# Kernel tuning notes

Measured on AMD Instinct MI355X. Metric: run time of the kernel, lower is better.

## Reference

```python
import jax, jax.numpy as jnp
import numpy as np

B, T, IN, H = 4096, 128, 768, 256


def setup_inputs() -> dict:
    key = jax.random.key(0)
    ks = jax.random.split(key, 5)
    s1 = 1.0 / np.sqrt(IN)
    s2 = 1.0 / np.sqrt(H)
    return {
        "x": jax.random.normal(ks[0], (B, IN), jnp.float32),
        "W1": jax.random.normal(ks[1], (T, IN, H), jnp.float32) * s1,
        "b1": jnp.zeros((T, H), jnp.float32),
        "W2": jax.random.normal(ks[2], (T, H, H), jnp.float32) * s2,
        "b2": jnp.zeros((T, H), jnp.float32),
        "W3": jax.random.normal(ks[3], (T, H), jnp.float32) * s2,
        "b3": jnp.zeros((T,), jnp.float32),
    }


def reference(x, W1, b1, W2, b2, W3, b3):
    # Per-task 3-layer MLP, vectorized over tasks. Dropout is eval-mode (identity).
    h = jax.nn.relu(jnp.einsum('bi,tih->bth', x, W1) + b1)          # [B, T, H]
    h = jax.nn.relu(jnp.einsum('bth,thk->btk', h, W2) + b2)         # [B, T, H]
    out = jnp.einsum('bth,th->bt', h, W3) + b3                      # [B, T]
    return out
```

## Files before the change

kernel.cpp:

```cpp
#include <hip/hip_runtime.h>
#include <cstdint>
#include <cstddef>

#define B_   4096
#define T_   128
#define IN_  768
#define H_   256
#define BM_  256
#define KC1  (IN_ / 32)
#define KC2  (H_ / 32)

typedef __bf16 bf16_t;
typedef bf16_t bf16x8 __attribute__((ext_vector_type(8)));
typedef bf16_t bf16x4 __attribute__((ext_vector_type(4)));
typedef float  floatx16 __attribute__((ext_vector_type(16)));

#define MFMA32(a, b, c) __builtin_amdgcn_mfma_f32_32x32x16_bf16((a), (b), (c), 0, 0, 0)

#define WAITBAR(N) asm volatile("s_waitcnt vmcnt(" #N ") lgkmcnt(0)\n\ts_barrier" ::: "memory")
#define WAIT_LGK_BAR() asm volatile("s_waitcnt lgkmcnt(0)\n\ts_barrier" ::: "memory")

__device__ __forceinline__ void gl_lds16(const bf16_t* g, bf16_t* l) {
    __builtin_amdgcn_global_load_lds(
        (const __attribute__((address_space(1))) void*)g,
        (__attribute__((address_space(3))) void*)l, 16, 0, 0);
}

__device__ __forceinline__ void tile_w_body(const float* __restrict__ src,
                                            bf16_t* __restrict__ dst,
                                            int K, int KC, int blk) {
    const int t  = blk / KC;
    const int kc = blk - t * KC;
    const int kq = threadIdx.x >> 6;
    const int h4 = (threadIdx.x & 63) * 4;
    const float* s = src + ((size_t)t * K + kc * 32 + kq * 8) * H_ + h4;
    float r[8][4];
#pragma unroll
    for (int e = 0; e < 8; ++e) {
        float4 v = *(const float4*)(s + (size_t)e * H_);
        r[e][0] = v.x; r[e][1] = v.y; r[e][2] = v.z; r[e][3] = v.w;
    }
    bf16_t* d = dst + (((size_t)(t * KC + kc) * 4 + kq) * H_ + h4) * 8;
#pragma unroll
    for (int c = 0; c < 4; ++c) {
        bf16x8 v;
#pragma unroll
        for (int e = 0; e < 8; ++e) v[e] = (bf16_t)r[e][c];
        *(bf16x8*)(d + c * 8) = v;
    }
}

__device__ __forceinline__ void tile_x_body(const float* __restrict__ src,
                                            bf16_t* __restrict__ dst, long long o) {
    int m = (int)(o & 127);
    long long q = o >> 7;
    int kq = (int)(q & 3);
    int q2 = (int)(q >> 2);
    int kc   = q2 % KC1;
    int mblk = q2 / KC1;
    const float* s = src + ((long long)mblk * 128 + m) * IN_ + kc * 32 + kq * 8;
    float4 a = *(const float4*)s;
    float4 b = *(const float4*)(s + 4);
    bf16x8 v;
    v[0] = (bf16_t)a.x; v[1] = (bf16_t)a.y; v[2] = (bf16_t)a.z; v[3] = (bf16_t)a.w;
    v[4] = (bf16_t)b.x; v[5] = (bf16_t)b.y; v[6] = (bf16_t)b.z; v[7] = (bf16_t)b.w;
    *(bf16x8*)(dst + o * 8) = v;
}

__global__ __launch_bounds__(256)
void prep_all(const float* __restrict__ x,  bf16_t* __restrict__ xt,
              const float* __restrict__ W1, bf16_t* __restrict__ w1t,
              const float* __restrict__ W2, bf16_t* __restrict__ w2t) {
    const int b = blockIdx.x;
    if (b < 1536) {
        long long o = (long long)b * 256 + threadIdx.x;
        tile_x_body(x, xt, o);
    } else if (b < 1536 + 3072) {
        tile_w_body(W1, w1t, IN_, KC1, b - 1536);
    } else {
        tile_w_body(W2, w2t, H_, KC2, b - 4608);
    }
}

__global__ __launch_bounds__(512, 2)
void mtmlp_fused5(const bf16_t* __restrict__ xt, const bf16_t* __restrict__ w1t,
                  const float* __restrict__ b1, const bf16_t* __restrict__ w2t,
                  const float* __restrict__ b2, const float* __restrict__ W3,
                  const float* __restrict__ b3, float* __restrict__ out) {
    const int L    = blockIdx.x;
    const int xcd  = L & 7;
    const int slot = L >> 3;
    const int t    = xcd * 16 + (slot >> 4);
    const int mblk = slot & 15;
    const int m0   = mblk * BM_;
    const int mb0  = mblk * 2;

    const int tid  = threadIdx.x;
    const int lane = tid & 63;
    const int wid  = tid >> 6;
    const int wm   = wid >> 2;
    const int wn   = wid & 3;
    const int ln31 = lane & 31;
    const int hi   = lane >> 5;

    __shared__ __align__(16) bf16_t hbuf[BM_ * H_];
    __shared__ __align__(16) bf16_t wt2[2 * 4 * H_ * 8];
    float* w3s = (float*)wt2;

    floatx16 acc[4][2];
#pragma unroll
    for (int i = 0; i < 4; ++i)
#pragma unroll
        for (int j = 0; j < 2; ++j)
#pragma unroll
            for (int e = 0; e < 16; ++e) acc[i][j][e] = 0.0f;

    const bf16_t* w1base = w1t + (size_t)t * KC1 * 8192;
    const bf16_t* w2base = w2t + (size_t)t * KC2 * 8192;
    const bf16_t* xw = xt + (size_t)(mb0 + (wn >> 1)) * KC1 * 4096;
    const int lbase = hi * 1024 + (wn & 1) * 512 + ln31 * 8;
    const int abase = hi * 2048 + wm * 1024 + ln31 * 8;

    bf16_t* const sl0 = hbuf;
    bf16_t* const sl1 = hbuf + 8192;
    bf16_t* const sl2 = hbuf + 16384;
    bf16_t* const sl3 = hbuf + 24576;

    auto stageW = [&](bf16_t* dst, int kc) {
        const bf16_t* ws = w1base + (size_t)kc * 8192;
        gl_lds16(ws + tid * 8,        dst + tid * 8);
        gl_lds16(ws + 4096 + tid * 8, dst + 4096 + tid * 8);
    };
    auto stage2 = [&](bf16_t* dst, int kc) {
        const bf16_t* ws = w2base + (size_t)kc * 8192;
        gl_lds16(ws + tid * 8,        dst + tid * 8);
        gl_lds16(ws + 4096 + tid * 8, dst + 4096 + tid * 8);
    };

#define LOADX(XV, kcc) do {                                          \
        const bf16_t* xp_ = xw + (size_t)(kcc) * 4096;               \
        XV##0 = *(const bf16x8*)(xp_ + lbase + 0 * 2048 + 0 * 256);  \
        XV##1 = *(const bf16x8*)(xp_ + lbase + 0 * 2048 + 1 * 256);  \
        XV##2 = *(const bf16x8*)(xp_ + lbase + 1 * 2048 + 0 * 256);  \
        XV##3 = *(const bf16x8*)(xp_ + lbase + 1 * 2048 + 1 * 256);  \
    } while (0)

#define COMP1(bp_, XV) do {                                          \
        const bf16_t* b_ = (bp_);                                    \
        bf16x8 A0_, A1_, A2_, A3_;                                   \
        A0_ = *(const bf16x8*)(b_ + abase + 0 * 4096 + 0 * 256);     \
        A1_ = *(const bf16x8*)(b_ + abase + 0 * 4096 + 1 * 256);     \
        A2_ = *(const bf16x8*)(b_ + abase + 0 * 4096 + 2 * 256);     \
        A3_ = *(const bf16x8*)(b_ + abase + 0 * 4096 + 3 * 256);     \
        acc[0][0] = MFMA32(A0_, XV##0, acc[0][0]);                   \
        acc[0][1] = MFMA32(A0_, XV##1, acc[0][1]);                   \
        acc[1][0] = MFMA32(A1_, XV##0, acc[1][0]);                   \
        acc[1][1] = MFMA32(A1_, XV##1, acc[1][1]);                   \
        acc[2][0] = MFMA32(A2_, XV##0, acc[2][0]);                   \
        acc[2][1] = MFMA32(A2_, XV##1, acc[2][1]);                   \
        acc[3][0] = MFMA32(A3_, XV##0, acc[3][0]);                   \
        acc[3][1] = MFMA32(A3_, XV##1, acc[3][1]);                   \
        A0_ = *(const bf16x8*)(b_ + abase + 1 * 4096 + 0 * 256);     \
        A1_ = *(const bf16x8*)(b_ + abase + 1 * 4096 + 1 * 256);     \
        A2_ = *(const bf16x8*)(b_ + abase + 1 * 4096 + 2 * 256);     \
        A3_ = *(const bf16x8*)(b_ + abase + 1 * 4096 + 3 * 256);     \
        acc[0][0] = MFMA32(A0_, XV##2, acc[0][0]);                   \
        acc[0][1] = MFMA32(A0_, XV##3, acc[0][1]);                   \
        acc[1][0] = MFMA32(A1_, XV##2, acc[1][0]);                   \
        acc[1][1] = MFMA32(A1_, XV##3, acc[1][1]);                   \
        acc[2][0] = MFMA32(A2_, XV##2, acc[2][0]);                   \
        acc[2][1] = MFMA32(A2_, XV##3, acc[2][1]);                   \
        acc[3][0] = MFMA32(A3_, XV##2, acc[3][0]);                   \
        acc[3][1] = MFMA32(A3_, XV##3, acc[3][1]);                   \
    } while (0)

    bf16x8 xA0, xA1, xA2, xA3, xB0, xB1, xB2, xB3;

    stageW(sl0, 0); stageW(sl1, 1); stageW(sl2, 2);
    LOADX(xA, 0); LOADX(xB, 1);

    WAITBAR(4); stageW(sl3, 3); COMP1(sl0, xA); LOADX(xA, 2);
    WAITBAR(6); stageW(sl0, 4); COMP1(sl1, xB); LOADX(xB, 3);
    WAITBAR(6); stageW(sl1, 5); COMP1(sl2, xA); LOADX(xA, 4);
    WAITBAR(6); stageW(sl2, 6); COMP1(sl3, xB); LOADX(xB, 5);

    for (int q = 1; q <= 4; ++q) {
        const int kc = q * 4;
        WAITBAR(6); stageW(sl3, kc + 3); COMP1(sl0, xA); LOADX(xA, kc + 2);
        WAITBAR(6); stageW(sl0, kc + 4); COMP1(sl1, xB); LOADX(xB, kc + 3);
        WAITBAR(6); stageW(sl1, kc + 5); COMP1(sl2, xA); LOADX(xA, kc + 4);
        WAITBAR(6); stageW(sl2, kc + 6); COMP1(sl3, xB); LOADX(xB, kc + 5);
    }
    WAITBAR(6); stageW(sl3, 23); COMP1(sl0, xA); LOADX(xA, 22);
    WAITBAR(6);                  COMP1(sl1, xB); LOADX(xB, 23);
    WAITBAR(4); stage2(wt2, 0); stage2(wt2 + 8192, 1); COMP1(sl2, xA);
    WAITBAR(4);                  COMP1(sl3, xB);
    WAIT_LGK_BAR();

#pragma unroll
    for (int i = 0; i < 4; ++i) {
#pragma unroll
        for (int g = 0; g < 4; ++g) {
            const int h0 = wm * 128 + i * 32 + g * 8 + 4 * hi;
            float4 bias = *(const float4*)(b1 + t * H_ + h0);
            const int blk = h0 >> 3;
#pragma unroll
            for (int j = 0; j < 2; ++j) {
                const int mm = wn * 64 + j * 32 + ln31;
                bf16x4 o;
                o[0] = (bf16_t)fmaxf(acc[i][j][4 * g + 0] + bias.x, 0.0f);
                o[1] = (bf16_t)fmaxf(acc[i][j][4 * g + 1] + bias.y, 0.0f);
                o[2] = (bf16_t)fmaxf(acc[i][j][4 * g + 2] + bias.z, 0.0f);
                o[3] = (bf16_t)fmaxf(acc[i][j][4 * g + 3] + bias.w, 0.0f);
                *(bf16x4*)(hbuf + (size_t)(blk * BM_ + mm) * 8 + 4 * hi) = o;
            }
        }
    }

#pragma unroll
    for (int i = 0; i < 4; ++i)
#pragma unroll
        for (int j = 0; j < 2; ++j)
#pragma unroll
            for (int e = 0; e < 16; ++e) acc[i][j][e] = 0.0f;

    auto comp2 = [&](const bf16_t* wbuf, int kc) {
#pragma unroll
        for (int s = 0; s < 2; ++s) {
            const int kq = s * 2 + hi;
            bf16x8 A[4], Bf[2];
#pragma unroll
            for (int i = 0; i < 4; ++i)
                A[i] = *(const bf16x8*)(wbuf + (size_t)(kq * H_ + wm * 128 + i * 32 + ln31) * 8);
            const int blk = kc * 4 + kq;
#pragma unroll
            for (int j = 0; j < 2; ++j) {
                const int mm = wn * 64 + j * 32 + ln31;
                Bf[j] = *(const bf16x8*)(hbuf + (size_t)(blk * BM_ + mm) * 8);
            }
#pragma unroll
            for (int i = 0; i < 4; ++i)
#pragma unroll
                for (int j = 0; j < 2; ++j) acc[i][j] = MFMA32(A[i], Bf[j], acc[i][j]);
        }
    };

    for (int kc = 0; kc < KC2; ++kc) {
        if (kc < KC2 - 1) { WAITBAR(2); } else { WAITBAR(0); }
        comp2(wt2 + (kc & 1) * 8192, kc);
        WAIT_LGK_BAR();
        if (kc < KC2 - 2) stage2(wt2 + (kc & 1) * 8192, kc + 2);
    }

    if (tid < H_) w3s[tid] = W3[t * H_ + tid];
#pragma unroll
    for (int i = 0; i < 4; ++i) {
#pragma unroll
        for (int g = 0; g < 4; ++g) {
            const int h0 = wm * 128 + i * 32 + g * 8 + 4 * hi;
            float4 bias = *(const float4*)(b2 + t * H_ + h0);
            const int blk = h0 >> 3;
#pragma unroll
            for (int j = 0; j < 2; ++j) {
                const int mm = wn * 64 + j * 32 + ln31;
                bf16x4 o;
                o[0] = (bf16_t)fmaxf(acc[i][j][4 * g + 0] + bias.x, 0.0f);
                o[1] = (bf16_t)fmaxf(acc[i][j][4 * g + 1] + bias.y, 0.0f);
                o[2] = (bf16_t)fmaxf(acc[i][j][4 * g + 2] + bias.z, 0.0f);
                o[3] = (bf16_t)fmaxf(acc[i][j][4 * g + 3] + bias.w, 0.0f);
                *(bf16x4*)(hbuf + (size_t)(blk * BM_ + mm) * 8 + 4 * hi) = o;
            }
        }
    }
    WAIT_LGK_BAR();

    {
        const int m = tid >> 1, seg = tid & 1;
        float sum = 0.0f;
#pragma unroll
        for (int b = 0; b < 16; ++b) {
            const int blk = seg * 16 + b;
            const bf16x8 v = *(const bf16x8*)(hbuf + (size_t)(blk * BM_ + m) * 8);
            const float* w = w3s + blk * 8;
#pragma unroll
            for (int e = 0; e < 8; ++e) sum += (float)v[e] * w[e];
        }
        sum += __shfl_xor(sum, 1);
        if (seg == 0) out[(size_t)(m0 + m) * T_ + t] = sum + b3[t];
    }
#undef LOADX
#undef COMP1
}

extern "C" void kernel_launch(void* const* d_in, const int* in_sizes, int n_in,
                              void* d_out, int out_size, void* d_ws, size_t ws_size,
                              hipStream_t stream) {
    const float* x  = (const float*)d_in[0];
    const float* W1 = (const float*)d_in[1];
    const float* b1 = (const float*)d_in[2];
    const float* W2 = (const float*)d_in[3];
    const float* b2 = (const float*)d_in[4];
    const float* W3 = (const float*)d_in[5];
    const float* b3 = (const float*)d_in[6];
    float* out = (float*)d_out;

    const size_t nx  = (size_t)B_ * IN_;
    const size_t nw1 = (size_t)T_ * IN_ * H_;

    bf16_t* xt  = (bf16_t*)d_ws;
    bf16_t* w1t = xt + nx;
    bf16_t* w2t = w1t + nw1;

    prep_all<<<dim3(5632), 256, 0, stream>>>(x, xt, W1, w1t, W2, w2t);
    mtmlp_fused5<<<dim3(2048), 512, 0, stream>>>(xt, w1t, b1, w2t, b2, W3, b3, out);
}
```

Before: 456.8 us.

## Restage layer-1 W1 in paired triple buffers and stream layer-2 weights from registers

Layer 1 now stages two K-chunks of W1 per step into three 16K-element LDS slots (P0/P1/P2), so there are half as many barriers per K. Layer 2 no longer stages W2 through LDS. Each wave loads its own W2 fragments straight from global into double-buffered registers, and only the hidden activations are read from LDS. This removes the separate wt2 LDS buffer and the barriers around it, which shrinks LDS use. The cost is more registers and global-load latency that is no longer hidden behind barriers, plus less prefetch lead in layer 1.

Result: slower. 488.0 us (+6.8%).

```diff
diff --git a/kernel.cpp b/kernel.cpp
--- a/kernel.cpp
+++ b/kernel.cpp
@@ -83,7 +83,7 @@
 }
 
 __global__ __launch_bounds__(512, 2)
-void mtmlp_fused5(const bf16_t* __restrict__ xt, const bf16_t* __restrict__ w1t,
+void mtmlp_fused6(const bf16_t* __restrict__ xt, const bf16_t* __restrict__ w1t,
                   const float* __restrict__ b1, const bf16_t* __restrict__ w2t,
                   const float* __restrict__ b2, const float* __restrict__ W3,
                   const float* __restrict__ b3, float* __restrict__ out) {
@@ -104,8 +104,7 @@
     const int hi   = lane >> 5;
 
     __shared__ __align__(16) bf16_t hbuf[BM_ * H_];
-    __shared__ __align__(16) bf16_t wt2[2 * 4 * H_ * 8];
-    float* w3s = (float*)wt2;
+    __shared__ float w3s[H_];
 
     floatx16 acc[4][2];
 #pragma unroll
@@ -120,21 +119,19 @@
     const bf16_t* xw = xt + (size_t)(mb0 + (wn >> 1)) * KC1 * 4096;
     const int lbase = hi * 1024 + (wn & 1) * 512 + ln31 * 8;
     const int abase = hi * 2048 + wm * 1024 + ln31 * 8;
-
-    bf16_t* const sl0 = hbuf;
-    bf16_t* const sl1 = hbuf + 8192;
-    bf16_t* const sl2 = hbuf + 16384;
-    bf16_t* const sl3 = hbuf + 24576;
-
-    auto stageW = [&](bf16_t* dst, int kc) {
+    const int mm0 = wn * 64 + ln31;
+    const int mm1 = mm0 + 32;
+
+    bf16_t* const P0 = hbuf;
+    bf16_t* const P1 = hbuf + 16384;
+    bf16_t* const P2 = hbuf + 32768;
+
+    auto stageWpair = [&](bf16_t* dst, int kc) {
         const bf16_t* ws = w1base + (size_t)kc * 8192;
-        gl_lds16(ws + tid * 8,        dst + tid * 8);
-        gl_lds16(ws + 4096 + tid * 8, dst + 4096 + tid * 8);
-    };
-    auto stage2 = [&](bf16_t* dst, int kc) {
-        const bf16_t* ws = w2base + (size_t)kc * 8192;
-        gl_lds16(ws + tid * 8,        dst + tid * 8);
-        gl_lds16(ws + 4096 + tid * 8, dst + 4096 + tid * 8);
+        gl_lds16(ws + tid * 8,         dst + tid * 8);
+        gl_lds16(ws + 4096 + tid * 8,  dst + 4096 + tid * 8);
+        gl_lds16(ws + 8192 + tid * 8,  dst + 8192 + tid * 8);
+        gl_lds16(ws + 12288 + tid * 8, dst + 12288 + tid * 8);
     };
 
 #define LOADX(XV, kcc) do {                                          \
@@ -174,27 +171,35 @@
         acc[3][1] = MFMA32(A3_, XV##3, acc[3][1]);                   \
     } while (0)
 
-    bf16x8 xA0, xA1, xA2, xA3, xB0, xB1, xB2, xB3;
-
-    stageW(sl0, 0); stageW(sl1, 1); stageW(sl2, 2);
-    LOADX(xA, 0); LOADX(xB, 1);
-
-    WAITBAR(4); stageW(sl3, 3); COMP1(sl0, xA); LOADX(xA, 2);
-    WAITBAR(6); stageW(sl0, 4); COMP1(sl1, xB); LOADX(xB, 3);
-    WAITBAR(6); stageW(sl1, 5); COMP1(sl2, xA); LOADX(xA, 4);
-    WAITBAR(6); stageW(sl2, 6); COMP1(sl3, xB); LOADX(xB, 5);
-
-    for (int q = 1; q <= 4; ++q) {
-        const int kc = q * 4;
-        WAITBAR(6); stageW(sl3, kc + 3); COMP1(sl0, xA); LOADX(xA, kc + 2);
-        WAITBAR(6); stageW(sl0, kc + 4); COMP1(sl1, xB); LOADX(xB, kc + 3);
-        WAITBAR(6); stageW(sl1, kc + 5); COMP1(sl2, xA); LOADX(xA, kc + 4);
-        WAITBAR(6); stageW(sl2, kc + 6); COMP1(sl3, xB); LOADX(xB, kc + 5);
-    }
-    WAITBAR(6); stageW(sl3, 23); COMP1(sl0, xA); LOADX(xA, 22);
-    WAITBAR(6);                  COMP1(sl1, xB); LOADX(xB, 23);
-    WAITBAR(4); stage2(wt2, 0); stage2(wt2 + 8192, 1); COMP1(sl2, xA);
-    WAITBAR(4);                  COMP1(sl3, xB);
+#define SUPER(CB, WB, XUa, XUb, XNa, XNb, c) do {                    \
+        WAITBAR(4);                                                  \
+        LOADX(XNa, (c) + 2); LOADX(XNb, (c) + 3);                    \
+        stageWpair(WB, (c) + 4);                                     \
+        COMP1(CB, XUa); COMP1((CB) + 8192, XUb);                     \
+    } while (0)
+
+    bf16x8 xPA0, xPA1, xPA2, xPA3, xPB0, xPB1, xPB2, xPB3;
+    bf16x8 xQA0, xQA1, xQA2, xQA3, xQB0, xQB1, xQB2, xQB3;
+
+    LOADX(xPA, 0); LOADX(xPB, 1);
+    stageWpair(P0, 0);
+    stageWpair(P1, 2);
+
+    SUPER(P0, P2, xPA, xPB, xQA, xQB, 0);
+    SUPER(P1, P0, xQA, xQB, xPA, xPB, 2);
+    SUPER(P2, P1, xPA, xPB, xQA, xQB, 4);
+    SUPER(P0, P2, xQA, xQB, xPA, xPB, 6);
+    SUPER(P1, P0, xPA, xPB, xQA, xQB, 8);
+    SUPER(P2, P1, xQA, xQB, xPA, xPB, 10);
+    SUPER(P0, P2, xPA, xPB, xQA, xQB, 12);
+    SUPER(P1, P0, xQA, xQB, xPA, xPB, 14);
+    SUPER(P2, P1, xPA, xPB, xQA, xQB, 16);
+    SUPER(P0, P2, xQA, xQB, xPA, xPB, 18);
+    WAITBAR(4);
+    LOADX(xQA, 22); LOADX(xQB, 23);
+    COMP1(P1, xPA); COMP1(P1 + 8192, xPB);
+    WAITBAR(0);
+    COMP1(P2, xQA); COMP1(P2 + 8192, xQB);
     WAIT_LGK_BAR();
 
 #pragma unroll
@@ -224,33 +229,61 @@
 #pragma unroll
             for (int e = 0; e < 16; ++e) acc[i][j][e] = 0.0f;
 
-    auto comp2 = [&](const bf16_t* wbuf, int kc) {
-#pragma unroll
-        for (int s = 0; s < 2; ++s) {
-            const int kq = s * 2 + hi;
-            bf16x8 A[4], Bf[2];
-#pragma unroll
-            for (int i = 0; i < 4; ++i)
-                A[i] = *(const bf16x8*)(wbuf + (size_t)(kq * H_ + wm * 128 + i * 32 + ln31) * 8);
-            const int blk = kc * 4 + kq;
-#pragma unroll
-            for (int j = 0; j < 2; ++j) {
-                const int mm = wn * 64 + j * 32 + ln31;
-                Bf[j] = *(const bf16x8*)(hbuf + (size_t)(blk * BM_ + mm) * 8);
-            }
-#pragma unroll
-            for (int i = 0; i < 4; ++i)
-#pragma unroll
-                for (int j = 0; j < 2; ++j) acc[i][j] = MFMA32(A[i], Bf[j], acc[i][j]);
-        }
-    };
-
-    for (int kc = 0; kc < KC2; ++kc) {
-        if (kc < KC2 - 1) { WAITBAR(2); } else { WAITBAR(0); }
-        comp2(wt2 + (kc & 1) * 8192, kc);
-        WAIT_LGK_BAR();
-        if (kc < KC2 - 2) stage2(wt2 + (kc & 1) * 8192, kc + 2);
-    }
+    WAIT_LGK_BAR();
+
+#define LOADW2(WV, kcc) do {                                         \
+        const bf16_t* wp_ = w2base + (size_t)(kcc) * 8192;           \
+        WV##0 = *(const bf16x8*)(wp_ + abase + 0 * 4096 + 0 * 256);  \
+        WV##1 = *(const bf16x8*)(wp_ + abase + 0 * 4096 + 1 * 256);  \
+        WV##2 = *(const bf16x8*)(wp_ + abase + 0 * 4096 + 2 * 256);  \
+        WV##3 = *(const bf16x8*)(wp_ + abase + 0 * 4096 + 3 * 256);  \
+        WV##4 = *(const bf16x8*)(wp_ + abase + 1 * 4096 + 0 * 256);  \
+        WV##5 = *(const bf16x8*)(wp_ + abase + 1 * 4096 + 1 * 256);  \
+        WV##6 = *(const bf16x8*)(wp_ + abase + 1 * 4096 + 2 * 256);  \
+        WV##7 = *(const bf16x8*)(wp_ + abase + 1 * 4096 + 3 * 256);  \
+    } while (0)
+
+#define COMP2R(WV, kcc) do {                                         \
+        bf16x8 B0_, B1_;                                             \
+        const int blkA_ = (kcc) * 4 + hi;                            \
+        B0_ = *(const bf16x8*)(hbuf + (size_t)(blkA_ * BM_ + mm0) * 8); \
+        B1_ = *(const bf16x8*)(hbuf + (size_t)(blkA_ * BM_ + mm1) * 8); \
+        acc[0][0] = MFMA32(WV##0, B0_, acc[0][0]);                   \
+        acc[0][1] = MFMA32(WV##0, B1_, acc[0][1]);                   \
+        acc[1][0] = MFMA32(WV##1, B0_, acc[1][0]);                   \
+        acc[1][1] = MFMA32(WV##1, B1_, acc[1][1]);                   \
+        acc[2][0] = MFMA32(WV##2, B0_, acc[2][0]);                   \
+        acc[2][1] = MFMA32(WV##2, B1_, acc[2][1]);                   \
+        acc[3][0] = MFMA32(WV##3, B0_, acc[3][0]);                   \
+        acc[3][1] = MFMA32(WV##3, B1_, acc[3][1]);                   \
+        const int blkB_ = (kcc) * 4 + 2 + hi;                        \
+        B0_ = *(const bf16x8*)(hbuf + (size_t)(blkB_ * BM_ + mm0) * 8); \
+        B1_ = *(const bf16x8*)(hbuf + (size_t)(blkB_ * BM_ + mm1) * 8); \
+        acc[0][0] = MFMA32(WV##4, B0_, acc[0][0]);                   \
+        acc[0][1] = MFMA32(WV##4, B1_, acc[0][1]);                   \
+        acc[1][0] = MFMA32(WV##5, B0_, acc[1][0]);                   \
+        acc[1][1] = MFMA32(WV##5, B1_, acc[1][1]);                   \
+        acc[2][0] = MFMA32(WV##6, B0_, acc[2][0]);                   \
+        acc[2][1] = MFMA32(WV##6, B1_, acc[2][1]);                   \
+        acc[3][0] = MFMA32(WV##7, B0_, acc[3][0]);                   \
+        acc[3][1] = MFMA32(WV##7, B1_, acc[3][1]);                   \
+    } while (0)
+
+    {
+        bf16x8 wa0, wa1, wa2, wa3, wa4, wa5, wa6, wa7;
+        bf16x8 wb0, wb1, wb2, wb3, wb4, wb5, wb6, wb7;
+        LOADW2(wa, 0); LOADW2(wb, 1);
+        COMP2R(wa, 0); LOADW2(wa, 2);
+        COMP2R(wb, 1); LOADW2(wb, 3);
+        COMP2R(wa, 2); LOADW2(wa, 4);
+        COMP2R(wb, 3); LOADW2(wb, 5);
+        COMP2R(wa, 4); LOADW2(wa, 6);
+        COMP2R(wb, 5); LOADW2(wb, 7);
+        COMP2R(wa, 6);
+        COMP2R(wb, 7);
+    }
+
+    WAIT_LGK_BAR();
 
     if (tid < H_) w3s[tid] = W3[t * H_ + tid];
 #pragma unroll
@@ -290,6 +323,9 @@
     }
 #undef LOADX
 #undef COMP1
+#undef SUPER
+#undef LOADW2
+#undef COMP2R
 }
 
 extern "C" void kernel_launch(void* const* d_in, const int* in_sizes, int n_in,
@@ -312,5 +348,5 @@
     bf16_t* w2t = w1t + nw1;
 
     prep_all<<<dim3(5632), 256, 0, stream>>>(x, xt, W1, w1t, W2, w2t);
-    mtmlp_fused5<<<dim3(2048), 512, 0, stream>>>(xt, w1t, b1, w2t, b2, W3, b3, out);
-}
+    mtmlp_fused6<<<dim3(2048), 512, 0, stream>>>(xt, w1t, b1, w2t, b2, W3, b3, out);
+}
```

## Halve batch tile to 128, raise occupancy, stream W2 directly into registers

Applied to the files above, without the earlier changes.

Shrinks the per-block batch tile from 256 to 128 rows, doubling the grid and halving the accumulator registers so launch bounds can request four blocks per SIMD. The second-layer weights are now loaded straight from global memory into registers with double-buffering, instead of being staged through an LDS double buffer. The final dot product is split four ways per row. In exchange, each W1/W2 tile is fetched twice as often per batch row, and the register path for W2 loses the LDS sharing across waves.

Measured after the change: 484.0 us. 1.06x slower.

```diff
diff --git a/kernel.cpp b/kernel.cpp
--- a/kernel.cpp
+++ b/kernel.cpp
@@ -6,7 +6,7 @@
 #define T_   128
 #define IN_  768
 #define H_   256
-#define BM_  256
+#define BM_  128
 #define KC1  (IN_ / 32)
 #define KC2  (H_ / 32)
 
@@ -82,18 +82,17 @@
     }
 }
 
-__global__ __launch_bounds__(512, 2)
-void mtmlp_fused5(const bf16_t* __restrict__ xt, const bf16_t* __restrict__ w1t,
+__global__ __launch_bounds__(512, 4)
+void mtmlp_fused7(const bf16_t* __restrict__ xt, const bf16_t* __restrict__ w1t,
                   const float* __restrict__ b1, const bf16_t* __restrict__ w2t,
                   const float* __restrict__ b2, const float* __restrict__ W3,
                   const float* __restrict__ b3, float* __restrict__ out) {
     const int L    = blockIdx.x;
     const int xcd  = L & 7;
     const int slot = L >> 3;
-    const int t    = xcd * 16 + (slot >> 4);
-    const int mblk = slot & 15;
+    const int t    = xcd * 16 + (slot >> 5);
+    const int mblk = slot & 31;
     const int m0   = mblk * BM_;
-    const int mb0  = mblk * 2;
 
     const int tid  = threadIdx.x;
     const int lane = tid & 63;
@@ -104,22 +103,20 @@
     const int hi   = lane >> 5;
 
     __shared__ __align__(16) bf16_t hbuf[BM_ * H_];
-    __shared__ __align__(16) bf16_t wt2[2 * 4 * H_ * 8];
-    float* w3s = (float*)wt2;
-
-    floatx16 acc[4][2];
+    __shared__ float w3s[H_];
+
+    floatx16 acc[4];
 #pragma unroll
     for (int i = 0; i < 4; ++i)
 #pragma unroll
-        for (int j = 0; j < 2; ++j)
-#pragma unroll
-            for (int e = 0; e < 16; ++e) acc[i][j][e] = 0.0f;
+        for (int e = 0; e < 16; ++e) acc[i][e] = 0.0f;
 
     const bf16_t* w1base = w1t + (size_t)t * KC1 * 8192;
     const bf16_t* w2base = w2t + (size_t)t * KC2 * 8192;
-    const bf16_t* xw = xt + (size_t)(mb0 + (wn >> 1)) * KC1 * 4096;
-    const int lbase = hi * 1024 + (wn & 1) * 512 + ln31 * 8;
-    const int abase = hi * 2048 + wm * 1024 + ln31 * 8;
+    const bf16_t* xw = xt + (size_t)mblk * KC1 * 4096;
+    const int mmx  = wn * 32 + ln31;
+    const int xoff = hi * 1024 + mmx * 8;
+    const int aoff = hi * 2048 + wm * 1024 + ln31 * 8;
 
     bf16_t* const sl0 = hbuf;
     bf16_t* const sl1 = hbuf + 8192;
@@ -131,70 +128,63 @@
         gl_lds16(ws + tid * 8,        dst + tid * 8);
         gl_lds16(ws + 4096 + tid * 8, dst + 4096 + tid * 8);
     };
-    auto stage2 = [&](bf16_t* dst, int kc) {
-        const bf16_t* ws = w2base + (size_t)kc * 8192;
-        gl_lds16(ws + tid * 8,        dst + tid * 8);
-        gl_lds16(ws + 4096 + tid * 8, dst + 4096 + tid * 8);
-    };
 
 #define LOADX(XV, kcc) do {                                          \
         const bf16_t* xp_ = xw + (size_t)(kcc) * 4096;               \
-        XV##0 = *(const bf16x8*)(xp_ + lbase + 0 * 2048 + 0 * 256);  \
-        XV##1 = *(const bf16x8*)(xp_ + lbase + 0 * 2048 + 1 * 256);  \
-        XV##2 = *(const bf16x8*)(xp_ + lbase + 1 * 2048 + 0 * 256);  \
-        XV##3 = *(const bf16x8*)(xp_ + lbase + 1 * 2048 + 1 * 256);  \
+        XV##0 = *(const bf16x8*)(xp_ + xoff);                        \
+        XV##1 = *(const bf16x8*)(xp_ + xoff + 2048);                 \
     } while (0)
 
 #define COMP1(bp_, XV) do {                                          \
         const bf16_t* b_ = (bp_);                                    \
         bf16x8 A0_, A1_, A2_, A3_;                                   \
-        A0_ = *(const bf16x8*)(b_ + abase + 0 * 4096 + 0 * 256);     \
-        A1_ = *(const bf16x8*)(b_ + abase + 0 * 4096 + 1 * 256);     \
-        A2_ = *(const bf16x8*)(b_ + abase + 0 * 4096 + 2 * 256);     \
-        A3_ = *(const bf16x8*)(b_ + abase + 0 * 4096 + 3 * 256);     \
-        acc[0][0] = MFMA32(A0_, XV##0, acc[0][0]);                   \
-        acc[0][1] = MFMA32(A0_, XV##1, acc[0][1]);                   \
-        acc[1][0] = MFMA32(A1_, XV##0, acc[1][0]);                   \
-        acc[1][1] = MFMA32(A1_, XV##1, acc[1][1]);                   \
-        acc[2][0] = MFMA32(A2_, XV##0, acc[2][0]);                   \
-        acc[2][1] = MFMA32(A2_, XV##1, acc[2][1]);                   \
-        acc[3][0] = MFMA32(A3_, XV##0, acc[3][0]);                   \
-        acc[3][1] = MFMA32(A3_, XV##1, acc[3][1]);                   \
-        A0_ = *(const bf16x8*)(b_ + abase + 1 * 4096 + 0 * 256);     \
-        A1_ = *(const bf16x8*)(b_ + abase + 1 * 4096 + 1 * 256);     \
-        A2_ = *(const bf16x8*)(b_ + abase + 1 * 4096 + 2 * 256);     \
-        A3_ = *(const bf16x8*)(b_ + abase + 1 * 4096 + 3 * 256);     \
-        acc[0][0] = MFMA32(A0_, XV##2, acc[0][0]);                   \
-        acc[0][1] = MFMA32(A0_, XV##3, acc[0][1]);                   \
-        acc[1][0] = MFMA32(A1_, XV##2, acc[1][0]);                   \
-        acc[1][1] = MFMA32(A1_, XV##3, acc[1][1]);                   \
-        acc[2][0] = MFMA32(A2_, XV##2, acc[2][0]);                   \
-        acc[2][1] = MFMA32(A2_, XV##3, acc[2][1]);                   \
-        acc[3][0] = MFMA32(A3_, XV##2, acc[3][0]);                   \
-        acc[3][1] = MFMA32(A3_, XV##3, acc[3][1]);                   \
+        A0_ = *(const bf16x8*)(b_ + aoff + 0 * 256);                 \
+        A1_ = *(const bf16x8*)(b_ + aoff + 1 * 256);                 \
+        A2_ = *(const bf16x8*)(b_ + aoff + 2 * 256);                 \
+        A3_ = *(const bf16x8*)(b_ + aoff + 3 * 256);                 \
+        acc[0] = MFMA32(A0_, XV##0, acc[0]);                         \
+        acc[1] = MFMA32(A1_, XV##0, acc[1]);                         \
+        acc[2] = MFMA32(A2_, XV##0, acc[2]);                         \
+        acc[3] = MFMA32(A3_, XV##0, acc[3]);                         \
+        A0_ = *(const bf16x8*)(b_ + aoff + 4096 + 0 * 256);          \
+        A1_ = *(const bf16x8*)(b_ + aoff + 4096 + 1 * 256);          \
+        A2_ = *(const bf16x8*)(b_ + aoff + 4096 + 2 * 256);         \
+        A3_ = *(const bf16x8*)(b_ + aoff + 4096 + 3 * 256);          \
+        acc[0] = MFMA32(A0_, XV##1, acc[0]);                         \
+        acc[1] = MFMA32(A1_, XV##1, acc[1]);                         \
+        acc[2] = MFMA32(A2_, XV##1, acc[2]);                         \
+        acc[3] = MFMA32(A3_, XV##1, acc[3]);                         \
     } while (0)
 
-    bf16x8 xA0, xA1, xA2, xA3, xB0, xB1, xB2, xB3;
-
+    bf16x8 xA0, xA1, xB0, xB1;
+
+    LOADX(xA, 0); LOADX(xB, 1);
     stageW(sl0, 0); stageW(sl1, 1); stageW(sl2, 2);
-    LOADX(xA, 0); LOADX(xB, 1);
-
-    WAITBAR(4); stageW(sl3, 3); COMP1(sl0, xA); LOADX(xA, 2);
-    WAITBAR(6); stageW(sl0, 4); COMP1(sl1, xB); LOADX(xB, 3);
-    WAITBAR(6); stageW(sl1, 5); COMP1(sl2, xA); LOADX(xA, 4);
-    WAITBAR(6); stageW(sl2, 6); COMP1(sl3, xB); LOADX(xB, 5);
-
-    for (int q = 1; q <= 4; ++q) {
-        const int kc = q * 4;
-        WAITBAR(6); stageW(sl3, kc + 3); COMP1(sl0, xA); LOADX(xA, kc + 2);
-        WAITBAR(6); stageW(sl0, kc + 4); COMP1(sl1, xB); LOADX(xB, kc + 3);
-        WAITBAR(6); stageW(sl1, kc + 5); COMP1(sl2, xA); LOADX(xA, kc + 4);
-        WAITBAR(6); stageW(sl2, kc + 6); COMP1(sl3, xB); LOADX(xB, kc + 5);
-    }
-    WAITBAR(6); stageW(sl3, 23); COMP1(sl0, xA); LOADX(xA, 22);
-    WAITBAR(6);                  COMP1(sl1, xB); LOADX(xB, 23);
-    WAITBAR(4); stage2(wt2, 0); stage2(wt2 + 8192, 1); COMP1(sl2, xA);
-    WAITBAR(4);                  COMP1(sl3, xB);
+
+    WAITBAR(4); stageW(sl3, 3);  COMP1(sl0, xA); LOADX(xA, 2);
+    WAITBAR(6); stageW(sl0, 4);  COMP1(sl1, xB); LOADX(xB, 3);
+    WAITBAR(4); stageW(sl1, 5);  COMP1(sl2, xA); LOADX(xA, 4);
+    WAITBAR(4); stageW(sl2, 6);  COMP1(sl3, xB); LOADX(xB, 5);
+    WAITBAR(4); stageW(sl3, 7);  COMP1(sl0, xA); LOADX(xA, 6);
+    WAITBAR(4); stageW(sl0, 8);  COMP1(sl1, xB); LOADX(xB, 7);
+    WAITBAR(4); stageW(sl1, 9);  COMP1(sl2, xA); LOADX(xA, 8);
+    WAITBAR(4); stageW(sl2, 10); COMP1(sl3, xB); LOADX(xB, 9);
+    WAITBAR(4); stageW(sl3, 11); COMP1(sl0, xA); LOADX(xA, 10);
+    WAITBAR(4); stageW(sl0, 12); COMP1(sl1, xB); LOADX(xB, 11);
+    WAITBAR(4); stageW(sl1, 13); COMP1(sl2, xA); LOADX(xA, 12);
+    WAITBAR(4); stageW(sl2, 14); COMP1(sl3, xB); LOADX(xB, 13);
+    WAITBAR(4); stageW(sl3, 15); COMP1(sl0, xA); LOADX(xA, 14);
+    WAITBAR(4); stageW(sl0, 16); COMP1(sl1, xB); LOADX(xB, 15);
+    WAITBAR(4); stageW(sl1, 17); COMP1(sl2, xA); LOADX(xA, 16);
+    WAITBAR(4); stageW(sl2, 18); COMP1(sl3, xB); LOADX(xB, 17);
+    WAITBAR(4); stageW(sl3, 19); COMP1(sl0, xA); LOADX(xA, 18);
+    WAITBAR(4); stageW(sl0, 20); COMP1(sl1, xB); LOADX(xB, 19);
+    WAITBAR(4); stageW(sl1, 21); COMP1(sl2, xA); LOADX(xA, 20);
+    WAITBAR(4); stageW(sl2, 22); COMP1(sl3, xB); LOADX(xB, 21);
+    WAITBAR(4); stageW(sl3, 23); COMP1(sl0, xA); LOADX(xA, 22);
+    WAITBAR(4);                  COMP1(sl1, xB); LOADX(xB, 23);
+    WAITBAR(2);                  COMP1(sl2, xA);
+    WAITBAR(0);                  COMP1(sl3, xB);
     WAIT_LGK_BAR();
 
 #pragma unroll
@@ -204,53 +194,63 @@
             const int h0 = wm * 128 + i * 32 + g * 8 + 4 * hi;
             float4 bias = *(const float4*)(b1 + t * H_ + h0);
             const int blk = h0 >> 3;
-#pragma unroll
-            for (int j = 0; j < 2; ++j) {
-                const int mm = wn * 64 + j * 32 + ln31;
-                bf16x4 o;
-                o[0] = (bf16_t)fmaxf(acc[i][j][4 * g + 0] + bias.x, 0.0f);
-                o[1] = (bf16_t)fmaxf(acc[i][j][4 * g + 1] + bias.y, 0.0f);
-                o[2] = (bf16_t)fmaxf(acc[i][j][4 * g + 2] + bias.z, 0.0f);
-                o[3] = (bf16_t)fmaxf(acc[i][j][4 * g + 3] + bias.w, 0.0f);
-                *(bf16x4*)(hbuf + (size_t)(blk * BM_ + mm) * 8 + 4 * hi) = o;
-            }
+            bf16x4 o;
+            o[0] = (bf16_t)fmaxf(acc[i][4 * g + 0] + bias.x, 0.0f);
+            o[1] = (bf16_t)fmaxf(acc[i][4 * g + 1] + bias.y, 0.0f);
+            o[2] = (bf16_t)fmaxf(acc[i][4 * g + 2] + bias.z, 0.0f);
+            o[3] = (bf16_t)fmaxf(acc[i][4 * g + 3] + bias.w, 0.0f);
+            *(bf16x4*)(hbuf + (size_t)(blk * BM_ + mmx) * 8 + 4 * hi) = o;
         }
     }
 
 #pragma unroll
     for (int i = 0; i < 4; ++i)
 #pragma unroll
-        for (int j = 0; j < 2; ++j)
-#pragma unroll
-            for (int e = 0; e < 16; ++e) acc[i][j][e] = 0.0f;
-
-    auto comp2 = [&](const bf16_t* wbuf, int kc) {
-#pragma unroll
-        for (int s = 0; s < 2; ++s) {
-            const int kq = s * 2 + hi;
-            bf16x8 A[4], Bf[2];
-#pragma unroll
-            for (int i = 0; i < 4; ++i)
-                A[i] = *(const bf16x8*)(wbuf + (size_t)(kq * H_ + wm * 128 + i * 32 + ln31) * 8);
-            const int blk = kc * 4 + kq;
-#pragma unroll
-            for (int j = 0; j < 2; ++j) {
-                const int mm = wn * 64 + j * 32 + ln31;
-                Bf[j] = *(const bf16x8*)(hbuf + (size_t)(blk * BM_ + mm) * 8);
-            }
-#pragma unroll
-            for (int i = 0; i < 4; ++i)
-#pragma unroll
-                for (int j = 0; j < 2; ++j) acc[i][j] = MFMA32(A[i], Bf[j], acc[i][j]);
-        }
-    };
-
-    for (int kc = 0; kc < KC2; ++kc) {
-        if (kc < KC2 - 1) { WAITBAR(2); } else { WAITBAR(0); }
-        comp2(wt2 + (kc & 1) * 8192, kc);
-        WAIT_LGK_BAR();
-        if (kc < KC2 - 2) stage2(wt2 + (kc & 1) * 8192, kc + 2);
-    }
+        for (int e = 0; e < 16; ++e) acc[i][e] = 0.0f;
+
+    WAIT_LGK_BAR();
+
+#define LOADW2H(WV, ks) do {                                         \
+        const bf16_t* wp_ = w2base + ((ks) >> 1) * 8192              \
+                            + ((ks) & 1) * 4096 + aoff;              \
+        WV##0 = *(const bf16x8*)(wp_ + 0 * 256);                     \
+        WV##1 = *(const bf16x8*)(wp_ + 1 * 256);                     \
+        WV##2 = *(const bf16x8*)(wp_ + 2 * 256);                     \
+        WV##3 = *(const bf16x8*)(wp_ + 3 * 256);                     \
+    } while (0)
+
+#define COMP2H(WV, ks) do {                                          \
+        const bf16x8 Bf_ = *(const bf16x8*)(hbuf +                   \
+            (size_t)(((ks) * 2 + hi) * BM_ + mmx) * 8);              \
+        acc[0] = MFMA32(WV##0, Bf_, acc[0]);                         \
+        acc[1] = MFMA32(WV##1, Bf_, acc[1]);                         \
+        acc[2] = MFMA32(WV##2, Bf_, acc[2]);                         \
+        acc[3] = MFMA32(WV##3, Bf_, acc[3]);                         \
+    } while (0)
+
+    {
+        bf16x8 wa0, wa1, wa2, wa3;
+        bf16x8 wb0, wb1, wb2, wb3;
+        LOADW2H(wa, 0);  LOADW2H(wb, 1);
+        COMP2H(wa, 0);   LOADW2H(wa, 2);
+        COMP2H(wb, 1);   LOADW2H(wb, 3);
+        COMP2H(wa, 2);   LOADW2H(wa, 4);
+        COMP2H(wb, 3);   LOADW2H(wb, 5);
+        COMP2H(wa, 4);   LOADW2H(wa, 6);
+        COMP2H(wb, 5);   LOADW2H(wb, 7);
+        COMP2H(wa, 6);   LOADW2H(wa, 8);
+        COMP2H(wb, 7);   LOADW2H(wb, 9);
+        COMP2H(wa, 8);   LOADW2H(wa, 10);
+        COMP2H(wb, 9);   LOADW2H(wb, 11);
+        COMP2H(wa, 10);  LOADW2H(wa, 12);
+        COMP2H(wb, 11);  LOADW2H(wb, 13);
+        COMP2H(wa, 12);  LOADW2H(wa, 14);
+        COMP2H(wb, 13);  LOADW2H(wb, 15);
+        COMP2H(wa, 14);
+        COMP2H(wb, 15);
+    }
+
+    WAIT_LGK_BAR();
 
     if (tid < H_) w3s[tid] = W3[t * H_ + tid];
 #pragma unroll
@@ -260,36 +260,35 @@
             const int h0 = wm * 128 + i * 32 + g * 8 + 4 * hi;
             float4 bias = *(const float4*)(b2 + t * H_ + h0);
             const int blk = h0 >> 3;
-#pragma unroll
-            for (int j = 0; j < 2; ++j) {
-                const int mm = wn * 64 + j * 32 + ln31;
-                bf16x4 o;
-                o[0] = (bf16_t)fmaxf(acc[i][j][4 * g + 0] + bias.x, 0.0f);
-                o[1] = (bf16_t)fmaxf(acc[i][j][4 * g + 1] + bias.y, 0.0f);
-                o[2] = (bf16_t)fmaxf(acc[i][j][4 * g + 2] + bias.z, 0.0f);
-                o[3] = (bf16_t)fmaxf(acc[i][j][4 * g + 3] + bias.w, 0.0f);
-                *(bf16x4*)(hbuf + (size_t)(blk * BM_ + mm) * 8 + 4 * hi) = o;
-            }
+            bf16x4 o;
+            o[0] = (bf16_t)fmaxf(acc[i][4 * g + 0] + bias.x, 0.0f);
+            o[1] = (bf16_t)fmaxf(acc[i][4 * g + 1] + bias.y, 0.0f);
+            o[2] = (bf16_t)fmaxf(acc[i][4 * g + 2] + bias.z, 0.0f);
+            o[3] = (bf16_t)fmaxf(acc[i][4 * g + 3] + bias.w, 0.0f);
+            *(bf16x4*)(hbuf + (size_t)(blk * BM_ + mmx) * 8 + 4 * hi) = o;
         }
     }
     WAIT_LGK_BAR();
 
     {
-        const int m = tid >> 1, seg = tid & 1;
+        const int m = tid >> 2, seg = tid & 3;
         float sum = 0.0f;
 #pragma unroll
-        for (int b = 0; b < 16; ++b) {
-            const int blk = seg * 16 + b;
+        for (int b = 0; b < 8; ++b) {
+            const int blk = seg * 8 + b;
             const bf16x8 v = *(const bf16x8*)(hbuf + (size_t)(blk * BM_ + m) * 8);
             const float* w = w3s + blk * 8;
 #pragma unroll
             for (int e = 0; e < 8; ++e) sum += (float)v[e] * w[e];
         }
         sum += __shfl_xor(sum, 1);
+        sum += __shfl_xor(sum, 2);
         if (seg == 0) out[(size_t)(m0 + m) * T_ + t] = sum + b3[t];
     }
 #undef LOADX
 #undef COMP1
+#undef LOADW2H
+#undef COMP2H
 }
 
 extern "C" void kernel_launch(void* const* d_in, const int* in_sizes, int n_in,
@@ -312,5 +311,5 @@
     bf16_t* w2t = w1t + nw1;
 
     prep_all<<<dim3(5632), 256, 0, stream>>>(x, xt, W1, w1t, W2, w2t);
-    mtmlp_fused5<<<dim3(2048), 512, 0, stream>>>(xt, w1t, b1, w2t, b2, W3, b3, out);
-}
+    mtmlp_fused7<<<dim3(4096), 512, 0, stream>>>(xt, w1t, b1, w2t, b2, W3, b3, out);
+}
```
